# Performance work log

Hardware: AMD Instinct MI355X
Metric: run time of the kernel (lower is better)

Reference implementation:

```python
import jax, jax.numpy as jnp
import numpy as np
import math

B, S, D, V = 16, 512, 64, 32000
MAX_SEQ = 512
TEMP = 1.0
EPS = 1e-12


def setup_inputs() -> dict:
    key = jax.random.key(0)
    k0, k1, k2, k3, k4 = jax.random.split(key, 5)
    tokens = jax.random.randint(k0, (B, S), 0, V)
    token_emb = jax.random.normal(k1, (V, D), dtype=jnp.float32) * 0.02
    lin_w1 = jax.random.normal(k2, (D, D), dtype=jnp.float32) * (1.0 / math.sqrt(D))
    lin_w2 = jax.random.normal(k3, (D, D), dtype=jnp.float32) * (1.0 / math.sqrt(D))
    edge_scale = jnp.full((1,), 0.1, dtype=jnp.float32)  # nn.Parameter init 0.1
    out_w = jax.random.normal(k4, (V, D), dtype=jnp.float32) * 0.02
    return {"tokens": tokens, "token_emb": token_emb, "lin_w1": lin_w1,
            "lin_w2": lin_w2, "edge_scale": edge_scale, "out_w": out_w}


def _embed(tokens, token_emb):
    # polar positional components (seq_len <= max_seq_len branch)
    pos = jnp.arange(S, dtype=jnp.float32)
    thetas = 2.0 * math.pi * (pos / MAX_SEQ)
    rs = 0.3 + 0.6 * (pos / (MAX_SEQ - 1))
    e0 = (rs * jnp.cos(thetas))[None, :, None]          # [1,S,1]
    e1 = (rs * jnp.sin(thetas))[None, :, None]          # [1,S,1]
    tok = token_emb[tokens][:, :, : D - 2]              # [B,S,D-2]
    emb = jnp.concatenate([jnp.broadcast_to(e0, (tok.shape[0], S, 1)),
                           jnp.broadcast_to(e1, (tok.shape[0], S, 1)),
                           tok], axis=-1)               # [B,S,D]
    norms = jnp.sqrt(jnp.clip(jnp.einsum('bsd,bsd->bs', emb, emb), EPS, None))
    return emb / norms[:, :, None]


def _attention(emb):
    # pairwise Euclidean distance attention, diagonal distance zeroed
    n2 = jnp.einsum('bsd,bsd->bs', emb, emb)                      # [B,S]
    dots = jnp.einsum('bqd,bkd->bqk', emb, emb)                   # [B,S,S]
    sq = n2[:, :, None] + n2[:, None, :] - 2.0 * dots
    dist = jnp.sqrt(jnp.clip(sq, EPS, None))
    dist = dist * (1.0 - jnp.eye(S, dtype=dist.dtype))[None]      # eye_mask
    return jax.nn.softmax(-dist / TEMP, axis=-1)                  # [B,S,S]


def reference(tokens, token_emb, lin_w1, lin_w2, edge_scale, out_w):
    emb = _embed(tokens, token_emb)            # [B,S,D]
    attn = _attention(emb)                     # [B,S,S]
    h = emb
    for w in (lin_w1, lin_w2):
        # message passing: x_j -> lin(x_j), edge weight = attn * edge_scale,
        # scatter-add over all incoming edges == batched attn @ h
        h = edge_scale[0] * jnp.einsum('bqk,bkd->bqd', attn, h @ w.T)
    logits = jnp.einsum('bsd,vd->bsv', h, out_w)   # [B,S,V]
    return logits
```

## Files before the change

kernel.cpp:

```cpp
#include <hip/hip_runtime.h>
#include <hip/hip_bf16.h>


#define S_ 512
#define D_ 64
#define V_ 32000

typedef __attribute__((ext_vector_type(8))) __bf16 bf16x8;
typedef __attribute__((ext_vector_type(4))) float f32x4;

__device__ inline unsigned short f2bf(float x) {
    __hip_bfloat16 h = __float2bfloat16(x);
    return __builtin_bit_cast(unsigned short, h);
}

__global__ __launch_bounds__(256) void embed_wprime_kernel(const int* __restrict__ tokens,
                                                           const float* __restrict__ temb,
                                                           float* __restrict__ emb,
                                                           float* __restrict__ n2,
                                                           const float* __restrict__ outw,
                                                           const float* __restrict__ w2,
                                                           unsigned short* __restrict__ wb) {
    __shared__ float os[16][68];
    __shared__ float w2t[64][68];
    int bid = blockIdx.x;
    if (bid < 2048) {
        int row  = bid * 4 + (threadIdx.x >> 6);
        int lane = threadIdx.x & 63;
        int s    = row & (S_ - 1);
        int tok  = tokens[row];
        float val;
        if (lane < 2) {
            float fs    = (float)s;
            float theta = 6.283185307179586f * (fs * (1.0f / 512.0f));
            float r     = 0.3f + 0.6f * (fs * (1.0f / 511.0f));
            val = (lane == 0) ? r * cosf(theta) : r * sinf(theta);
        } else {
            val = temb[tok * D_ + lane - 2];
        }
        float ss = val * val;
#pragma unroll
        for (int off = 32; off; off >>= 1) ss += __shfl_xor(ss, off, 64);
        float nrm = sqrtf(fmaxf(ss, 1e-12f));
        float e   = val / nrm;
        emb[row * D_ + lane] = e;
        float nn = e * e;
#pragma unroll
        for (int off = 32; off; off >>= 1) nn += __shfl_xor(nn, off, 64);
        if (lane == 0) n2[row] = nn;
    } else {
        int r0 = (bid - 2048) * 16;
        int t  = threadIdx.x;
        {
            int r = t >> 4, c4 = (t & 15) * 4;
            *reinterpret_cast<float4*>(&os[r][c4]) =
                *reinterpret_cast<const float4*>(&outw[(size_t)(r0 + r) * D_ + c4]);
        }
#pragma unroll
        for (int j = 0; j < 4; ++j) {
            int f4 = t + j * 256;
            int d = f4 >> 4, c4 = (f4 & 15) * 4;
            float4 v = *reinterpret_cast<const float4*>(&w2[d * D_ + c4]);
            w2t[c4 + 0][d] = v.x; w2t[c4 + 1][d] = v.y;
            w2t[c4 + 2][d] = v.z; w2t[c4 + 3][d] = v.w;
        }
        __syncthreads();
        int q = t >> 4, eh = t & 15;
        f32x4 acc[4];
#pragma unroll
        for (int ej = 0; ej < 4; ++ej) acc[ej] = (f32x4){0.f, 0.f, 0.f, 0.f};
#pragma unroll
        for (int dc = 0; dc < 16; ++dc) {
            f32x4 ov = *reinterpret_cast<f32x4*>(&os[q][dc * 4]);
#pragma unroll
            for (int ej = 0; ej < 4; ++ej) {
                f32x4 wv = *reinterpret_cast<f32x4*>(&w2t[eh * 4 + ej][dc * 4]);
                acc[ej] += ov * wv;
            }
        }
        ushort4 r;
        r.x = f2bf((acc[0][0] + acc[0][1]) + (acc[0][2] + acc[0][3]));
        r.y = f2bf((acc[1][0] + acc[1][1]) + (acc[1][2] + acc[1][3]));
        r.z = f2bf((acc[2][0] + acc[2][1]) + (acc[2][2] + acc[2][3]));
        r.w = f2bf((acc[3][0] + acc[3][1]) + (acc[3][2] + acc[3][3]));
        *reinterpret_cast<ushort4*>(&wb[(size_t)(r0 + q) * D_ + eh * 4]) = r;
    }
}

__global__ __launch_bounds__(128) void attn_kernel(const float* __restrict__ emb,
                                                   const float* __restrict__ n2,
                                                   const float* __restrict__ edge_scale,
                                                   float* __restrict__ attn_u,
                                                   float* __restrict__ invs) {
    __shared__ float qs[16][68];
    __shared__ float ks[64][68];
    __shared__ float n2qs[16];
    __shared__ float n2ks[64];
    int b  = blockIdx.x >> 5;
    int q0 = (blockIdx.x & 31) * 16;
    int t  = threadIdx.x;
    const float* ebase = emb + (size_t)b * S_ * D_;
#pragma unroll
    for (int j = 0; j < 2; ++j) {
        int f4 = t + j * 128;
        int r = f4 >> 4, c4 = (f4 & 15) * 4;
        *reinterpret_cast<float4*>(&qs[r][c4]) =
            *reinterpret_cast<const float4*>(&ebase[(q0 + r) * D_ + c4]);
    }
    if (t < 16) n2qs[t] = n2[b * S_ + q0 + t];

    int qg = t >> 4;
    int kg = t & 15;
    float rs[2] = {0.f, 0.f};

    for (int kt = 0; kt < 8; ++kt) {
        int k0 = kt * 64;
        __syncthreads();
#pragma unroll
        for (int j = 0; j < 8; ++j) {
            int f4 = t + j * 128;
            int r = f4 >> 4, c4 = (f4 & 15) * 4;
            *reinterpret_cast<float4*>(&ks[r][c4]) =
                *reinterpret_cast<const float4*>(&ebase[(k0 + r) * D_ + c4]);
        }
        if (t < 64) n2ks[t] = n2[b * S_ + k0 + t];
        __syncthreads();

        f32x4 acc[2][4];
#pragma unroll
        for (int i = 0; i < 2; ++i)
#pragma unroll
            for (int j = 0; j < 4; ++j) acc[i][j] = (f32x4){0.f, 0.f, 0.f, 0.f};
#pragma unroll
        for (int dc = 0; dc < 16; ++dc) {
            f32x4 qv[2], kv[4];
#pragma unroll
            for (int i = 0; i < 2; ++i) qv[i] = *reinterpret_cast<f32x4*>(&qs[qg * 2 + i][dc * 4]);
#pragma unroll
            for (int j = 0; j < 4; ++j) kv[j] = *reinterpret_cast<f32x4*>(&ks[kg * 4 + j][dc * 4]);
#pragma unroll
            for (int i = 0; i < 2; ++i)
#pragma unroll
                for (int j = 0; j < 4; ++j) acc[i][j] += qv[i] * kv[j];
        }
#pragma unroll
        for (int i = 0; i < 2; ++i) {
            int q = qg * 2 + i;
            float4 ev;
            float* evp = &ev.x;
#pragma unroll
            for (int j = 0; j < 4; ++j) {
                int k = kg * 4 + j;
                f32x4 a = acc[i][j];
                float dot = (a[0] + a[1]) + (a[2] + a[3]);
                float sq  = n2qs[q] + n2ks[k] - 2.0f * dot;
                evp[j] = (q0 + q == k0 + k) ? 1.0f : __expf(-sqrtf(fmaxf(sq, 1e-12f)));
            }
            rs[i] += (ev.x + ev.y) + (ev.z + ev.w);
            *reinterpret_cast<float4*>(
                &attn_u[((size_t)(b * S_ + q0 + q)) * S_ + k0 + kg * 4]) = ev;
        }
    }
    float scale = edge_scale[0];
#pragma unroll
    for (int i = 0; i < 2; ++i) {
#pragma unroll
        for (int off = 1; off < 16; off <<= 1) rs[i] += __shfl_xor(rs[i], off, 64);
        if (kg == 0) invs[b * S_ + q0 + qg * 2 + i] = scale / rs[i];
    }
}

__global__ __launch_bounds__(128) void prop_proj_kernel(const float* __restrict__ attn_u,
                                                        const float* __restrict__ hsrc,
                                                        const float* __restrict__ w1,
                                                        const float* __restrict__ invs,
                                                        float* __restrict__ outf) {
    __shared__ float As[16][68];
    __shared__ float Ts[64][68];
    __shared__ float ws1[64][68];
    __shared__ float gs[16][68];
    int b  = blockIdx.x >> 5;
    int q0 = (blockIdx.x & 31) * 16;
    int t  = threadIdx.x;
    int qg = t >> 4, dh = t & 15;
#pragma unroll
    for (int j = 0; j < 8; ++j) {
        int f4 = t + j * 128;
        int r = f4 >> 4, c4 = (f4 & 15) * 4;
        *reinterpret_cast<float4*>(&ws1[r][c4]) =
            *reinterpret_cast<const float4*>(&w1[r * D_ + c4]);
    }
    f32x4 acc[2];
#pragma unroll
    for (int i = 0; i < 2; ++i) acc[i] = (f32x4){0.f, 0.f, 0.f, 0.f};
    const float* abase = attn_u + ((size_t)b * S_ + q0) * S_;
    const float* tbase = hsrc + (size_t)b * S_ * D_;
    for (int kt = 0; kt < 8; ++kt) {
        int k0 = kt * 64;
        __syncthreads();
#pragma unroll
        for (int j = 0; j < 2; ++j) {
            int f4 = t + j * 128;
            int r = f4 >> 4, c4 = (f4 & 15) * 4;
            *reinterpret_cast<float4*>(&As[r][c4]) =
                *reinterpret_cast<const float4*>(&abase[(size_t)r * S_ + k0 + c4]);
        }
#pragma unroll
        for (int j = 0; j < 8; ++j) {
            int f4 = t + j * 128;
            int r = f4 >> 4, c4 = (f4 & 15) * 4;
            *reinterpret_cast<float4*>(&Ts[r][c4]) =
                *reinterpret_cast<const float4*>(&tbase[(k0 + r) * D_ + c4]);
        }
        __syncthreads();
#pragma unroll
        for (int kc = 0; kc < 16; ++kc) {
            f32x4 tv[4];
#pragma unroll
            for (int ks = 0; ks < 4; ++ks)
                tv[ks] = *reinterpret_cast<f32x4*>(&Ts[kc * 4 + ks][dh * 4]);
#pragma unroll
            for (int i = 0; i < 2; ++i) {
                f32x4 av = *reinterpret_cast<f32x4*>(&As[qg * 2 + i][kc * 4]);
#pragma unroll
                for (int ks = 0; ks < 4; ++ks) acc[i] += av[ks] * tv[ks];
            }
        }
    }
#pragma unroll
    for (int i = 0; i < 2; ++i) {
        f32x4 v = acc[i];
        *reinterpret_cast<float4*>(&gs[qg * 2 + i][dh * 4]) =
            make_float4(v[0], v[1], v[2], v[3]);
    }
    __syncthreads();
    f32x4 acc2[2][4];
#pragma unroll
    for (int i = 0; i < 2; ++i)
#pragma unroll
        for (int dj = 0; dj < 4; ++dj) acc2[i][dj] = (f32x4){0.f, 0.f, 0.f, 0.f};
#pragma unroll
    for (int dc = 0; dc < 16; ++dc) {
        f32x4 wv[4];
#pragma unroll
        for (int dj = 0; dj < 4; ++dj)
            wv[dj] = *reinterpret_cast<f32x4*>(&ws1[dh * 4 + dj][dc * 4]);
#pragma unroll
        for (int i = 0; i < 2; ++i) {
            f32x4 gv = *reinterpret_cast<f32x4*>(&gs[qg * 2 + i][dc * 4]);
#pragma unroll
            for (int dj = 0; dj < 4; ++dj) acc2[i][dj] += gv * wv[dj];
        }
    }
#pragma unroll
    for (int i = 0; i < 2; ++i) {
        int row = b * S_ + q0 + qg * 2 + i;
        float inv = invs[row];
        float4 r;
        r.x = inv * ((acc2[i][0][0] + acc2[i][0][1]) + (acc2[i][0][2] + acc2[i][0][3]));
        r.y = inv * ((acc2[i][1][0] + acc2[i][1][1]) + (acc2[i][1][2] + acc2[i][1][3]));
        r.z = inv * ((acc2[i][2][0] + acc2[i][2][1]) + (acc2[i][2][2] + acc2[i][2][3]));
        r.w = inv * ((acc2[i][3][0] + acc2[i][3][1]) + (acc2[i][3][2] + acc2[i][3][3]));
        *reinterpret_cast<float4*>(&outf[(size_t)row * D_ + dh * 4]) = r;
    }
}

__global__ __launch_bounds__(128) void prop_kernel(const float* __restrict__ attn_u,
                                                   const float* __restrict__ tmat,
                                                   const float* __restrict__ invs,
                                                   unsigned short* __restrict__ outb) {
    __shared__ float As[16][68];
    __shared__ float Ts[64][68];
    int b  = blockIdx.x >> 5;
    int q0 = (blockIdx.x & 31) * 16;
    int t  = threadIdx.x;
    int qg = t >> 4, dh = t & 15;
    f32x4 acc[2];
#pragma unroll
    for (int i = 0; i < 2; ++i) acc[i] = (f32x4){0.f, 0.f, 0.f, 0.f};
    const float* abase = attn_u + ((size_t)b * S_ + q0) * S_;
    const float* tbase = tmat + (size_t)b * S_ * D_;
    for (int kt = 0; kt < 8; ++kt) {
        int k0 = kt * 64;
        __syncthreads();
#pragma unroll
        for (int j = 0; j < 2; ++j) {
            int f4 = t + j * 128;
            int r = f4 >> 4, c4 = (f4 & 15) * 4;
            *reinterpret_cast<float4*>(&As[r][c4]) =
                *reinterpret_cast<const float4*>(&abase[(size_t)r * S_ + k0 + c4]);
        }
#pragma unroll
        for (int j = 0; j < 8; ++j) {
            int f4 = t + j * 128;
            int r = f4 >> 4, c4 = (f4 & 15) * 4;
            *reinterpret_cast<float4*>(&Ts[r][c4]) =
                *reinterpret_cast<const float4*>(&tbase[(k0 + r) * D_ + c4]);
        }
        __syncthreads();
#pragma unroll
        for (int kc = 0; kc < 16; ++kc) {
            f32x4 tv[4];
#pragma unroll
            for (int ks = 0; ks < 4; ++ks)
                tv[ks] = *reinterpret_cast<f32x4*>(&Ts[kc * 4 + ks][dh * 4]);
#pragma unroll
            for (int i = 0; i < 2; ++i) {
                f32x4 av = *reinterpret_cast<f32x4*>(&As[qg * 2 + i][kc * 4]);
#pragma unroll
                for (int ks = 0; ks < 4; ++ks) acc[i] += av[ks] * tv[ks];
            }
        }
    }
#pragma unroll
    for (int i = 0; i < 2; ++i) {
        int row = b * S_ + q0 + qg * 2 + i;
        float inv = invs[row];
        ushort4 r;
        r.x = f2bf(inv * acc[i][0]); r.y = f2bf(inv * acc[i][1]);
        r.z = f2bf(inv * acc[i][2]); r.w = f2bf(inv * acc[i][3]);
        *reinterpret_cast<ushort4*>(&outb[(size_t)row * D_ + dh * 4]) = r;
    }
}

__global__ __launch_bounds__(256) void logits_kernel(const unsigned short* __restrict__ hb,
                                                     const unsigned short* __restrict__ wb,
                                                     float* __restrict__ out) {
    __shared__ float Ct[2][16][260];
    int bid = blockIdx.x;
    int nt = bid % 125, mt = bid / 125;
    int n0 = nt * 256, m0 = mt * 128;
    int wave = threadIdx.x >> 6, lane = threadIdx.x & 63;
    int lr = lane & 15, lh = lane >> 4;

    bf16x8 a[2][2][2];
#pragma unroll
    for (int c = 0; c < 2; ++c)
#pragma unroll
        for (int ns = 0; ns < 2; ++ns)
#pragma unroll
            for (int kh = 0; kh < 2; ++kh)
                a[c][ns][kh] = *reinterpret_cast<const bf16x8*>(
                    wb + (size_t)(n0 + wave * 64 + c * 32 + ns * 16 + lr) * D_ + kh * 32 + lh * 8);

    for (int ms = 0; ms < 8; ++ms) {
        const unsigned short* hrow = hb + (size_t)(m0 + ms * 16 + lr) * D_ + lh * 8;
        bf16x8 b0 = *reinterpret_cast<const bf16x8*>(hrow);
        bf16x8 b1 = *reinterpret_cast<const bf16x8*>(hrow + 32);
        f32x4 acc[2][2];
#pragma unroll
        for (int c = 0; c < 2; ++c)
#pragma unroll
            for (int ns = 0; ns < 2; ++ns) {
                acc[c][ns] = (f32x4){0.f, 0.f, 0.f, 0.f};
                acc[c][ns] = __builtin_amdgcn_mfma_f32_16x16x32_bf16(a[c][ns][0], b0, acc[c][ns], 0, 0, 0);
                acc[c][ns] = __builtin_amdgcn_mfma_f32_16x16x32_bf16(a[c][ns][1], b1, acc[c][ns], 0, 0, 0);
            }

        float* Lw = &Ct[ms & 1][lr][wave * 64];
#pragma unroll
        for (int c = 0; c < 2; ++c)
#pragma unroll
            for (int ns = 0; ns < 2; ++ns) {
                f32x4 v = acc[c][ns];
                *reinterpret_cast<float4*>(Lw + c * 32 + ns * 16 + lh * 4) =
                    make_float4(v[0], v[1], v[2], v[3]);
            }
        __syncthreads();

#pragma unroll
        for (int j = 0; j < 4; ++j) {
            int row = wave * 4 + j;
            const float* Lr = &Ct[ms & 1][row][lane * 4];
            float4 v = *reinterpret_cast<const float4*>(Lr);
            *reinterpret_cast<float4*>(out + (size_t)(m0 + ms * 16 + row) * V_ + n0 + lane * 4) = v;
        }
    }
}

extern "C" void kernel_launch(void* const* d_in, const int* in_sizes, int n_in,
                              void* d_out, int out_size, void* d_ws, size_t ws_size,
                              hipStream_t stream) {
    const int*   tokens = (const int*)d_in[0];
    const float* temb   = (const float*)d_in[1];
    const float* w1     = (const float*)d_in[2];
    const float* w2     = (const float*)d_in[3];
    const float* escale = (const float*)d_in[4];
    const float* outw   = (const float*)d_in[5];
    float*       out    = (float*)d_out;

    char* tail = (char*)d_out + 1048576000ull - 23068672ull;
    float* attn = (float*)(tail);
    float* emb  = (float*)(tail + 16777216);
    float* h1   = (float*)(tail + 18874368);

    char* ws = (char*)d_ws;
    unsigned short* hb   = (unsigned short*)(ws);
    unsigned short* wb   = (unsigned short*)(ws + 1048576);
    float*          n2   = (float*)(ws + 5144576);
    float*          invs = (float*)(ws + 5177344);

    embed_wprime_kernel<<<4048, 256, 0, stream>>>(tokens, temb, emb, n2, outw, w2, wb);
    attn_kernel<<<512, 128, 0, stream>>>(emb, n2, escale, attn, invs);
    prop_proj_kernel<<<512, 128, 0, stream>>>(attn, emb, w1, invs, h1);
    prop_kernel<<<512, 128, 0, stream>>>(attn, h1, invs, hb);
    logits_kernel<<<8000, 256, 0, stream>>>(hb, wb, out);
}
```

Measured before the change: 294.6 us.

## Fuse attention computation with first propagation and projection step

Merges the attention kernel and the first prop_proj kernel. Each block keeps its 16x512 unnormalized attention rows in shared memory and reuses them for attn@emb followed by the W1 projection. This removes a kernel launch and the global re-read of the attention tile. The attention matrix is still written out for the second propagation. Shared memory per block grows to roughly 60KB, which may lower occupancy. The emb key tiles are reloaded a second time.

```diff
diff --git a/kernel.cpp b/kernel.cpp
--- a/kernel.cpp
+++ b/kernel.cpp
@@ -87,15 +87,21 @@
     }
 }
 
-__global__ __launch_bounds__(128) void attn_kernel(const float* __restrict__ emb,
-                                                   const float* __restrict__ n2,
-                                                   const float* __restrict__ edge_scale,
-                                                   float* __restrict__ attn_u,
-                                                   float* __restrict__ invs) {
+__global__ __launch_bounds__(128) void attn_prop_kernel(const float* __restrict__ emb,
+                                                        const float* __restrict__ n2,
+                                                        const float* __restrict__ edge_scale,
+                                                        const float* __restrict__ w1,
+                                                        float* __restrict__ attn_u,
+                                                        float* __restrict__ invs,
+                                                        float* __restrict__ h1) {
     __shared__ float qs[16][68];
     __shared__ float ks[64][68];
+    __shared__ float sc[16][520];
+    __shared__ float ws1[64][68];
+    __shared__ float gs[16][68];
     __shared__ float n2qs[16];
     __shared__ float n2ks[64];
+    __shared__ float invl[16];
     int b  = blockIdx.x >> 5;
     int q0 = (blockIdx.x & 31) * 16;
     int t  = threadIdx.x;
@@ -106,6 +112,13 @@
         int r = f4 >> 4, c4 = (f4 & 15) * 4;
         *reinterpret_cast<float4*>(&qs[r][c4]) =
             *reinterpret_cast<const float4*>(&ebase[(q0 + r) * D_ + c4]);
+    }
+#pragma unroll
+    for (int j = 0; j < 8; ++j) {
+        int f4 = t + j * 128;
+        int r = f4 >> 4, c4 = (f4 & 15) * 4;
+        *reinterpret_cast<float4*>(&ws1[r][c4]) =
+            *reinterpret_cast<const float4*>(&w1[r * D_ + c4]);
     }
     if (t < 16) n2qs[t] = n2[b * S_ + q0 + t];
 
@@ -157,6 +170,7 @@
                 evp[j] = (q0 + q == k0 + k) ? 1.0f : __expf(-sqrtf(fmaxf(sq, 1e-12f)));
             }
             rs[i] += (ev.x + ev.y) + (ev.z + ev.w);
+            *reinterpret_cast<float4*>(&sc[q][k0 + kg * 4]) = ev;
             *reinterpret_cast<float4*>(
                 &attn_u[((size_t)(b * S_ + q0 + q)) * S_ + k0 + kg * 4]) = ev;
         }
@@ -166,70 +180,45 @@
     for (int i = 0; i < 2; ++i) {
 #pragma unroll
         for (int off = 1; off < 16; off <<= 1) rs[i] += __shfl_xor(rs[i], off, 64);
-        if (kg == 0) invs[b * S_ + q0 + qg * 2 + i] = scale / rs[i];
-    }
-}
-
-__global__ __launch_bounds__(128) void prop_proj_kernel(const float* __restrict__ attn_u,
-                                                        const float* __restrict__ hsrc,
-                                                        const float* __restrict__ w1,
-                                                        const float* __restrict__ invs,
-                                                        float* __restrict__ outf) {
-    __shared__ float As[16][68];
-    __shared__ float Ts[64][68];
-    __shared__ float ws1[64][68];
-    __shared__ float gs[16][68];
-    int b  = blockIdx.x >> 5;
-    int q0 = (blockIdx.x & 31) * 16;
-    int t  = threadIdx.x;
-    int qg = t >> 4, dh = t & 15;
-#pragma unroll
-    for (int j = 0; j < 8; ++j) {
-        int f4 = t + j * 128;
-        int r = f4 >> 4, c4 = (f4 & 15) * 4;
-        *reinterpret_cast<float4*>(&ws1[r][c4]) =
-            *reinterpret_cast<const float4*>(&w1[r * D_ + c4]);
-    }
-    f32x4 acc[2];
-#pragma unroll
-    for (int i = 0; i < 2; ++i) acc[i] = (f32x4){0.f, 0.f, 0.f, 0.f};
-    const float* abase = attn_u + ((size_t)b * S_ + q0) * S_;
-    const float* tbase = hsrc + (size_t)b * S_ * D_;
+        if (kg == 0) {
+            float v = scale / rs[i];
+            invs[b * S_ + q0 + qg * 2 + i] = v;
+            invl[qg * 2 + i] = v;
+        }
+    }
+
+    int dh = kg;
+    f32x4 g[2];
+#pragma unroll
+    for (int i = 0; i < 2; ++i) g[i] = (f32x4){0.f, 0.f, 0.f, 0.f};
     for (int kt = 0; kt < 8; ++kt) {
         int k0 = kt * 64;
         __syncthreads();
-#pragma unroll
-        for (int j = 0; j < 2; ++j) {
-            int f4 = t + j * 128;
-            int r = f4 >> 4, c4 = (f4 & 15) * 4;
-            *reinterpret_cast<float4*>(&As[r][c4]) =
-                *reinterpret_cast<const float4*>(&abase[(size_t)r * S_ + k0 + c4]);
-        }
 #pragma unroll
         for (int j = 0; j < 8; ++j) {
             int f4 = t + j * 128;
             int r = f4 >> 4, c4 = (f4 & 15) * 4;
-            *reinterpret_cast<float4*>(&Ts[r][c4]) =
-                *reinterpret_cast<const float4*>(&tbase[(k0 + r) * D_ + c4]);
+            *reinterpret_cast<float4*>(&ks[r][c4]) =
+                *reinterpret_cast<const float4*>(&ebase[(k0 + r) * D_ + c4]);
         }
         __syncthreads();
 #pragma unroll
         for (int kc = 0; kc < 16; ++kc) {
             f32x4 tv[4];
 #pragma unroll
-            for (int ks = 0; ks < 4; ++ks)
-                tv[ks] = *reinterpret_cast<f32x4*>(&Ts[kc * 4 + ks][dh * 4]);
+            for (int ksl = 0; ksl < 4; ++ksl)
+                tv[ksl] = *reinterpret_cast<f32x4*>(&ks[kc * 4 + ksl][dh * 4]);
 #pragma unroll
             for (int i = 0; i < 2; ++i) {
-                f32x4 av = *reinterpret_cast<f32x4*>(&As[qg * 2 + i][kc * 4]);
-#pragma unroll
-                for (int ks = 0; ks < 4; ++ks) acc[i] += av[ks] * tv[ks];
+                f32x4 av = *reinterpret_cast<f32x4*>(&sc[qg * 2 + i][k0 + kc * 4]);
+#pragma unroll
+                for (int ksl = 0; ksl < 4; ++ksl) g[i] += av[ksl] * tv[ksl];
             }
         }
     }
 #pragma unroll
     for (int i = 0; i < 2; ++i) {
-        f32x4 v = acc[i];
+        f32x4 v = g[i];
         *reinterpret_cast<float4*>(&gs[qg * 2 + i][dh * 4]) =
             make_float4(v[0], v[1], v[2], v[3]);
     }
@@ -255,13 +244,13 @@
 #pragma unroll
     for (int i = 0; i < 2; ++i) {
         int row = b * S_ + q0 + qg * 2 + i;
-        float inv = invs[row];
+        float inv = invl[qg * 2 + i];
         float4 r;
         r.x = inv * ((acc2[i][0][0] + acc2[i][0][1]) + (acc2[i][0][2] + acc2[i][0][3]));
         r.y = inv * ((acc2[i][1][0] + acc2[i][1][1]) + (acc2[i][1][2] + acc2[i][1][3]));
         r.z = inv * ((acc2[i][2][0] + acc2[i][2][1]) + (acc2[i][2][2] + acc2[i][2][3]));
         r.w = inv * ((acc2[i][3][0] + acc2[i][3][1]) + (acc2[i][3][2] + acc2[i][3][3]));
-        *reinterpret_cast<float4*>(&outf[(size_t)row * D_ + dh * 4]) = r;
+        *reinterpret_cast<float4*>(&h1[(size_t)row * D_ + dh * 4]) = r;
     }
 }
 
@@ -401,8 +390,7 @@
     float*          invs = (float*)(ws + 5177344);
 
     embed_wprime_kernel<<<4048, 256, 0, stream>>>(tokens, temb, emb, n2, outw, w2, wb);
-    attn_kernel<<<512, 128, 0, stream>>>(emb, n2, escale, attn, invs);
-    prop_proj_kernel<<<512, 128, 0, stream>>>(attn, emb, w1, invs, h1);
+    attn_prop_kernel<<<512, 128, 0, stream>>>(emb, n2, escale, w1, attn, invs, h1);
     prop_kernel<<<512, 128, 0, stream>>>(attn, h1, invs, hb);
     logits_kernel<<<8000, 256, 0, stream>>>(hb, wb, out);
 }
```

New measurement: 297.7 us. Within noise of the previous version (+1.1%).
